# Kernel optimization log

Measured on AMD Instinct MI355X. Metric: run time of the kernel, lower is better.

## Reference

```python
import jax, jax.numpy as jnp
import numpy as np

N_NODES = 100000


def _gcn_norm(edge_index, edge_weight, num_nodes):
    # add self loops with weight 1 (PyG GCNConv default)
    loop = jnp.arange(num_nodes, dtype=edge_index.dtype)
    src = jnp.concatenate([edge_index[0], loop])
    dst = jnp.concatenate([edge_index[1], loop])
    w = jnp.concatenate([edge_weight, jnp.ones(num_nodes, edge_weight.dtype)])
    deg = jax.ops.segment_sum(w, dst, num_segments=num_nodes)
    dinv = jnp.where(deg > 0, jax.lax.rsqrt(deg), 0.0).astype(edge_weight.dtype)
    norm = dinv[src] * w * dinv[dst]
    return src, dst, norm


def _gcn_conv(x, W, b, src, dst, norm):
    h = x @ W                                   # [N, out]
    msg = h[src] * norm[:, None]                # [E+N, out] gather + scale
    out = jax.ops.segment_sum(msg, dst, num_segments=x.shape[0])
    return out + b


def setup_inputs() -> dict:
    key = jax.random.key(0)
    ks = jax.random.split(key, 6)
    nfeat, nhid, nclass, E = 128, 64, 40, 1600000
    return {
        "x": jax.random.normal(ks[0], (N_NODES, nfeat), jnp.float32),
        "edge_index": jax.random.randint(ks[1], (2, E), 0, N_NODES, jnp.int64),
        "edge_weight": jax.random.uniform(ks[2], (E,), jnp.float32),
        "W1": jax.random.normal(ks[3], (nfeat, nhid), jnp.float32) / np.sqrt(nfeat),
        "b1": jnp.zeros((nhid,), jnp.float32),
        "W2": jax.random.normal(ks[4], (nhid, nclass), jnp.float32) / np.sqrt(nhid),
        "b2": jnp.zeros((nclass,), jnp.float32),
    }


def reference(x, edge_index, edge_weight, W1, b1, W2, b2):
    src, dst, norm = _gcn_norm(edge_index, edge_weight, x.shape[0])
    h = jax.nn.relu(_gcn_conv(x, W1, b1, src, dst, norm))
    # dropout p=0.0 / eval mode -> identity
    h = _gcn_conv(h, W2, b2, src, dst, norm)
    return jax.nn.log_softmax(h, axis=1)
```

## Files before the change

kernel.cpp:

```cpp
#include <hip/hip_runtime.h>
#include <hip/hip_fp16.h>
#include <math.h>

#define NFEAT 128
#define NHID 64
#define NCLASS 40
#define BNODES 256
#define BSHIFT 8
#define EPB 4096
#define CAPSH 13
#define CAP (1 << CAPSH)
#define LCAP 5120

typedef _Float16 f16x8 __attribute__((ext_vector_type(8)));
typedef float f32x4 __attribute__((ext_vector_type(4)));

static __device__ __forceinline__ __half2 i2h2(int x) { union { int i; __half2 h; } u; u.i = x; return u.h; }
static __device__ __forceinline__ int h22i(__half2 h) { union { int i; __half2 h; } u; u.h = h; return u.i; }
static __device__ __forceinline__ __half2 shfl_xor_h2(__half2 v, int off) { return i2h2(__shfl_xor(h22i(v), off)); }


__global__ void k_init(int* __restrict__ gcur, int NB) {
    int i = blockIdx.x * blockDim.x + threadIdx.x;
    if (i < NB) gcur[i] = i << CAPSH;
}

__global__ __launch_bounds__(256) void k_bscatter(const int* __restrict__ src, const int* __restrict__ dst,
                                                  const float* __restrict__ w, int* __restrict__ gcur,
                                                  int2* __restrict__ csrT, int E, int NB) {
    __shared__ int lcnt[512], lbase[512], lpos[512];
    int t = threadIdx.x;
    for (int i = t; i < NB; i += 256) { lcnt[i] = 0; lpos[i] = 0; }
    __syncthreads();
    int base = blockIdx.x * EPB;
    int rs[16], rd[16]; float rw[16];
    #pragma unroll
    for (int i = 0; i < 16; i++) {
        int e = base + t + i * 256;
        bool ok = (e < E);
        rd[i] = ok ? dst[e] : -1;
        rs[i] = ok ? src[e] : 0;
        rw[i] = ok ? w[e] : 0.f;
    }
    #pragma unroll
    for (int i = 0; i < 16; i++)
        if (rd[i] >= 0) atomicAdd(&lcnt[rd[i] >> BSHIFT], 1);
    __syncthreads();
    for (int i = t; i < NB; i += 256) if (lcnt[i]) lbase[i] = atomicAdd(&gcur[i], lcnt[i]);
    __syncthreads();
    #pragma unroll
    for (int i = 0; i < 16; i++) {
        if (rd[i] >= 0) {
            int d = rd[i];
            int b = d >> BSHIFT;
            int p = atomicAdd(&lpos[b], 1);
            int2 v;
            v.x = rs[i] | ((d & (BNODES - 1)) << 20);
            v.y = __float_as_int(rw[i]);
            csrT[lbase[b] + p] = v;
        }
    }
}

__global__ __launch_bounds__(512) void k_cscan(const int* __restrict__ gcur, int* __restrict__ cbase, int NB) {
    __shared__ int sh[512];
    int t = threadIdx.x;
    int c = (t < NB) ? (gcur[t] - (t << CAPSH)) : 0;
    sh[t] = c;
    __syncthreads();
    for (int off = 1; off < 512; off <<= 1) {
        int v = (t >= off) ? sh[t - off] : 0;
        __syncthreads();
        sh[t] += v;
        __syncthreads();
    }
    if (t < NB) cbase[t] = sh[t] - c;
}

__global__ __launch_bounds__(256) void k_lsort(const int* __restrict__ gcur, const int* __restrict__ cbase,
                                               const int2* __restrict__ csrT, int2* __restrict__ csr,
                                               int* __restrict__ offs, float* __restrict__ dinv,
                                               int N, int E) {
    __shared__ int2 sorted[LCAP];
    __shared__ int lh[BNODES];
    __shared__ int lo[BNODES];
    __shared__ float da[BNODES];
    int b = blockIdx.x, t = threadIdx.x;
    int rbase = b << CAPSH;
    int cnt = gcur[b] - rbase;
    if (cnt > LCAP) cnt = LCAP;
    int cb = cbase[b];
    lh[t] = 0; da[t] = 0.f;
    __syncthreads();
    int2 reg[20];
    #pragma unroll
    for (int i = 0; i < 20; i++) {
        int e = t + i * 256;
        reg[i] = (e < cnt) ? csrT[rbase + e] : make_int2(-1, 0);
    }
    #pragma unroll
    for (int i = 0; i < 20; i++) {
        if (reg[i].x >= 0) {
            int dl = (reg[i].x >> 20) & 255;
            atomicAdd(&lh[dl], 1);
            atomicAdd(&da[dl], __int_as_float(reg[i].y));
        }
    }
    __syncthreads();
    int own = lh[t];
    lo[t] = own;
    __syncthreads();
    for (int off = 1; off < 256; off <<= 1) {
        int v = (t >= off) ? lo[t - off] : 0;
        __syncthreads();
        lo[t] += v;
        __syncthreads();
    }
    int excl = lo[t] - own;
    __syncthreads();
    lh[t] = excl;
    int gn = (b << BSHIFT) + t;
    if (gn < N) {
        offs[gn] = cb + excl;
        dinv[gn] = rsqrtf(1.0f + da[t]);
    }
    if (b == 0 && t == 0) offs[N] = E;
    __syncthreads();
    #pragma unroll
    for (int i = 0; i < 20; i++) {
        if (reg[i].x >= 0) {
            int dl = (reg[i].x >> 20) & 255;
            int p = atomicAdd(&lh[dl], 1);
            sorted[p] = reg[i];
        }
    }
    __syncthreads();
    for (int e = t; e < cnt; e += 256) {
        int2 v = sorted[e];
        __half2 w2 = __half2half2(__float2half(__int_as_float(v.y)));
        v.x &= 0xFFFFF;
        v.y = h22i(w2);
        csr[cb + e] = v;
    }
}


__global__ __launch_bounds__(256) void k_gemm1(const float* __restrict__ x,
                                               const float* __restrict__ W,
                                               const float* __restrict__ dinv,
                                               __half* __restrict__ h, int N) {
    __shared__ _Float16 xh[64][136];
    __shared__ _Float16 Wt[64][136];
    int t = threadIdx.x;
    int row0 = blockIdx.x * 64;
    for (int i = t; i < 4096; i += 256) {
        int r = i >> 6, k2 = i & 63;
        int row = row0 + r;
        float2 v = (row < N) ? ((const float2*)(x + (size_t)row * NFEAT))[k2]
                             : make_float2(0.f, 0.f);
        *(__half2*)&xh[r][k2 * 2] = __floats2half2_rn(v.x, v.y);
    }
    for (int i = t; i < 4096; i += 256) {
        int k2 = i >> 6, c = i & 63;
        float a0 = W[(size_t)(2 * k2) * NHID + c];
        float a1 = W[(size_t)(2 * k2 + 1) * NHID + c];
        *(__half2*)&Wt[c][k2 * 2] = __floats2half2_rn(a0, a1);
    }
    __syncthreads();
    int wave = t >> 6, lane = t & 63;
    int quad = lane >> 4, l16 = lane & 15;
    int r0 = wave * 16;
    f32x4 acc[4] = {};
    #pragma unroll
    for (int k0 = 0; k0 < 128; k0 += 32) {
        f16x8 af = *(const f16x8*)&xh[r0 + l16][k0 + quad * 8];
        #pragma unroll
        for (int ct = 0; ct < 4; ct++) {
            f16x8 bf = *(const f16x8*)&Wt[ct * 16 + l16][k0 + quad * 8];
            acc[ct] = __builtin_amdgcn_mfma_f32_16x16x32_f16(af, bf, acc[ct], 0, 0, 0);
        }
    }
    #pragma unroll
    for (int ct = 0; ct < 4; ct++) {
        #pragma unroll
        for (int j = 0; j < 4; j++) {
            int row = row0 + r0 + quad * 4 + j;
            if (row < N)
                h[(size_t)row * NHID + ct * 16 + l16] = __float2half(dinv[row] * acc[ct][j]);
        }
    }
}


__global__ __launch_bounds__(256) void k_agg1(const int* __restrict__ offs, const int2* __restrict__ csr,
                                              const __half* __restrict__ h1, const float* __restrict__ dinv,
                                              const float* __restrict__ b1, __half* __restrict__ out1, int N) {
    int n = (blockIdx.x * blockDim.x + threadIdx.x) >> 6;
    if (n >= N) return;
    int lane = threadIdx.x & 63;
    int grp = lane >> 3;
    int c8 = lane & 7;
    const char* hb = (const char*)h1;
    unsigned int c16 = (unsigned int)c8 << 4;
    int e = offs[n], end = offs[n + 1];
    float di = dinv[n];
    float4 hsv = *(const float4*)(hb + (unsigned int)n * 128u + c16);
    float4 bb0 = ((const float4*)b1)[2 * c8];
    float4 bb1 = ((const float4*)b1)[2 * c8 + 1];
    __half2 z = __floats2half2_rn(0.f, 0.f);
    __half2 aA[4] = {z, z, z, z}, aB[4] = {z, z, z, z};
    for (; e + 16 <= end; e += 16) {
        int2 vA = csr[e + grp];
        int2 vB = csr[e + 8 + grp];
        float4 hA = *(const float4*)(hb + (unsigned int)(vA.x & 0xFFFFF) * 128u + c16);
        float4 hB = *(const float4*)(hb + (unsigned int)(vB.x & 0xFFFFF) * 128u + c16);
        __half2 wA = i2h2(vA.y), wB = i2h2(vB.y);
        const __half2* pA = (const __half2*)&hA;
        const __half2* pB = (const __half2*)&hB;
        #pragma unroll
        for (int q = 0; q < 4; q++) {
            aA[q] = __hfma2(wA, pA[q], aA[q]);
            aB[q] = __hfma2(wB, pB[q], aB[q]);
        }
    }
    if (e + 8 <= end) {
        int2 v = csr[e + grp];
        float4 hv = *(const float4*)(hb + (unsigned int)(v.x & 0xFFFFF) * 128u + c16);
        __half2 wv = i2h2(v.y);
        const __half2* p = (const __half2*)&hv;
        #pragma unroll
        for (int q = 0; q < 4; q++) aA[q] = __hfma2(wv, p[q], aA[q]);
        e += 8;
    }
    if (e + grp < end) {
        int2 v = csr[e + grp];
        float4 hv = *(const float4*)(hb + (unsigned int)(v.x & 0xFFFFF) * 128u + c16);
        __half2 wv = i2h2(v.y);
        const __half2* p = (const __half2*)&hv;
        #pragma unroll
        for (int q = 0; q < 4; q++) aB[q] = __hfma2(wv, p[q], aB[q]);
    }
    __half2 acc2[4];
    #pragma unroll
    for (int q = 0; q < 4; q++) acc2[q] = __hadd2(aA[q], aB[q]);
    #pragma unroll
    for (int off = 8; off <= 32; off <<= 1) {
        #pragma unroll
        for (int q = 0; q < 4; q++) acc2[q] = __hadd2(acc2[q], shfl_xor_h2(acc2[q], off));
    }
    if (grp == 0) {
        float a[8], s[8];
        #pragma unroll
        for (int q = 0; q < 4; q++) {
            float2 fa = __half22float2(acc2[q]);
            a[2 * q] = fa.x; a[2 * q + 1] = fa.y;
            float2 f = __half22float2(((const __half2*)&hsv)[q]);
            s[2 * q] = f.x; s[2 * q + 1] = f.y;
        }
        float o[8];
        o[0] = fmaxf(di * (a[0] + s[0]) + bb0.x, 0.f);
        o[1] = fmaxf(di * (a[1] + s[1]) + bb0.y, 0.f);
        o[2] = fmaxf(di * (a[2] + s[2]) + bb0.z, 0.f);
        o[3] = fmaxf(di * (a[3] + s[3]) + bb0.w, 0.f);
        o[4] = fmaxf(di * (a[4] + s[4]) + bb1.x, 0.f);
        o[5] = fmaxf(di * (a[5] + s[5]) + bb1.y, 0.f);
        o[6] = fmaxf(di * (a[6] + s[6]) + bb1.z, 0.f);
        o[7] = fmaxf(di * (a[7] + s[7]) + bb1.w, 0.f);
        float4 st;
        #pragma unroll
        for (int q = 0; q < 4; q++)
            ((__half2*)&st)[q] = __floats2half2_rn(o[2 * q], o[2 * q + 1]);
        ((float4*)out1)[(size_t)n * 8 + c8] = st;
    }
}


__global__ __launch_bounds__(256) void k_gemm2(const __half* __restrict__ a,
                                               const float* __restrict__ W,
                                               const float* __restrict__ dinv,
                                               __half* __restrict__ h, int N) {
    __shared__ _Float16 As[64][72];
    __shared__ _Float16 Bt[64][72];
    int t = threadIdx.x;
    int row0 = blockIdx.x * 64;
    for (int i = t; i < 512; i += 256) {
        int r = i >> 3, q = i & 7;
        int row = row0 + r;
        f16x8 v = {};
        if (row < N) v = *(const f16x8*)(a + (size_t)row * NHID + q * 8);
        *(f16x8*)&As[r][q * 8] = v;
    }
    for (int i = t; i < 4096; i += 256) {
        int c = i >> 6, k = i & 63;
        float wv = (c < NCLASS) ? W[k * NCLASS + c] : 0.f;
        Bt[c][k] = (_Float16)wv;
    }
    __syncthreads();
    int wave = t >> 6, lane = t & 63;
    int quad = lane >> 4, l16 = lane & 15;
    int r0 = wave * 16;
    f32x4 acc[4] = {};
    #pragma unroll
    for (int k0 = 0; k0 < 64; k0 += 32) {
        f16x8 af = *(const f16x8*)&As[r0 + l16][k0 + quad * 8];
        #pragma unroll
        for (int ct = 0; ct < 4; ct++) {
            f16x8 bf = *(const f16x8*)&Bt[ct * 16 + l16][k0 + quad * 8];
            acc[ct] = __builtin_amdgcn_mfma_f32_16x16x32_f16(af, bf, acc[ct], 0, 0, 0);
        }
    }
    #pragma unroll
    for (int ct = 0; ct < 4; ct++) {
        int col = ct * 16 + l16;
        #pragma unroll
        for (int j = 0; j < 4; j++) {
            int row = row0 + r0 + quad * 4 + j;
            if (row < N)
                h[((size_t)row << 6) + col] = __float2half(dinv[row] * acc[ct][j]);
        }
    }
}


__global__ __launch_bounds__(256) void k_agg2(const int* __restrict__ offs, const int2* __restrict__ csr,
                                              const __half* __restrict__ h2, const float* __restrict__ dinv,
                                              const float* __restrict__ b2, float* __restrict__ out, int N) {
    int n = (blockIdx.x * blockDim.x + threadIdx.x) >> 6;
    if (n >= N) return;
    int lane = threadIdx.x & 63;
    int grp = lane >> 3;
    int c8 = lane & 7;
    const char* hb = (const char*)h2;
    unsigned int c16 = (unsigned int)c8 << 4;
    int e = offs[n], end = offs[n + 1];
    bool act = (c8 < 5);
    float di = dinv[n];
    float4 hsv = *(const float4*)(hb + ((unsigned int)n << 7) + c16);
    float4 bb0 = {}, bb1 = {};
    if (act) {
        bb0 = ((const float4*)b2)[2 * c8];
        bb1 = ((const float4*)b2)[2 * c8 + 1];
    }
    __half2 z = __floats2half2_rn(0.f, 0.f);
    __half2 aA[4] = {z, z, z, z}, aB[4] = {z, z, z, z};
    for (; e + 16 <= end; e += 16) {
        int2 vA = csr[e + grp];
        int2 vB = csr[e + 8 + grp];
        float4 hA = *(const float4*)(hb + ((unsigned int)(vA.x & 0xFFFFF) << 7) + c16);
        float4 hB = *(const float4*)(hb + ((unsigned int)(vB.x & 0xFFFFF) << 7) + c16);
        __half2 wA = i2h2(vA.y), wB = i2h2(vB.y);
        const __half2* pA = (const __half2*)&hA;
        const __half2* pB = (const __half2*)&hB;
        #pragma unroll
        for (int q = 0; q < 4; q++) {
            aA[q] = __hfma2(wA, pA[q], aA[q]);
            aB[q] = __hfma2(wB, pB[q], aB[q]);
        }
    }
    if (e + 8 <= end) {
        int2 v = csr[e + grp];
        float4 hv = *(const float4*)(hb + ((unsigned int)(v.x & 0xFFFFF) << 7) + c16);
        __half2 wv = i2h2(v.y);
        const __half2* p = (const __half2*)&hv;
        #pragma unroll
        for (int q = 0; q < 4; q++) aA[q] = __hfma2(wv, p[q], aA[q]);
        e += 8;
    }
    if (e + grp < end) {
        int2 v = csr[e + grp];
        float4 hv = *(const float4*)(hb + ((unsigned int)(v.x & 0xFFFFF) << 7) + c16);
        __half2 wv = i2h2(v.y);
        const __half2* p = (const __half2*)&hv;
        #pragma unroll
        for (int q = 0; q < 4; q++) aB[q] = __hfma2(wv, p[q], aB[q]);
    }
    __half2 acc2[4];
    #pragma unroll
    for (int q = 0; q < 4; q++) acc2[q] = __hadd2(aA[q], aB[q]);
    #pragma unroll
    for (int off = 8; off <= 32; off <<= 1) {
        #pragma unroll
        for (int q = 0; q < 4; q++) acc2[q] = __hadd2(acc2[q], shfl_xor_h2(acc2[q], off));
    }
    float a[8], s[8];
    #pragma unroll
    for (int q = 0; q < 4; q++) {
        float2 fa = __half22float2(acc2[q]);
        a[2 * q] = fa.x; a[2 * q + 1] = fa.y;
        float2 f = __half22float2(((const __half2*)&hsv)[q]);
        s[2 * q] = f.x; s[2 * q + 1] = f.y;
    }
    float v[8];
    v[0] = di * (a[0] + s[0]) + bb0.x;
    v[1] = di * (a[1] + s[1]) + bb0.y;
    v[2] = di * (a[2] + s[2]) + bb0.z;
    v[3] = di * (a[3] + s[3]) + bb0.w;
    v[4] = di * (a[4] + s[4]) + bb1.x;
    v[5] = di * (a[5] + s[5]) + bb1.y;
    v[6] = di * (a[6] + s[6]) + bb1.z;
    v[7] = di * (a[7] + s[7]) + bb1.w;
    float m = -INFINITY;
    if (act) {
        #pragma unroll
        for (int k = 0; k < 8; k++) m = fmaxf(m, v[k]);
    }
    #pragma unroll
    for (int off = 1; off <= 4; off <<= 1) m = fmaxf(m, __shfl_xor(m, off));
    float ex = 0.f;
    if (act) {
        #pragma unroll
        for (int k = 0; k < 8; k++) ex += __expf(v[k] - m);
    }
    #pragma unroll
    for (int off = 1; off <= 4; off <<= 1) ex += __shfl_xor(ex, off);
    if (act && grp == 0) {
        float ls = __logf(ex);
        float4 o0, o1;
        o0.x = v[0] - m - ls; o0.y = v[1] - m - ls; o0.z = v[2] - m - ls; o0.w = v[3] - m - ls;
        o1.x = v[4] - m - ls; o1.y = v[5] - m - ls; o1.z = v[6] - m - ls; o1.w = v[7] - m - ls;
        float* op = out + (size_t)n * NCLASS + c8 * 8;
        *(float4*)op = o0;
        *(float4*)(op + 4) = o1;
    }
}


extern "C" void kernel_launch(void* const* d_in, const int* in_sizes, int n_in,
                              void* d_out, int out_size, void* d_ws, size_t ws_size,
                              hipStream_t stream) {
    const float* x  = (const float*)d_in[0];
    const int*   ei = (const int*)d_in[1];
    const float* w  = (const float*)d_in[2];
    const float* W1 = (const float*)d_in[3];
    const float* b1 = (const float*)d_in[4];
    const float* W2 = (const float*)d_in[5];
    const float* b2 = (const float*)d_in[6];
    float* out = (float*)d_out;

    const int N = in_sizes[0] / NFEAT;
    const int E = in_sizes[1] / 2;
    const int* src = ei;
    const int* dst = ei + E;

    const int NB = (N + BNODES - 1) >> BSHIFT;
    const int nbuild = (E + EPB - 1) / EPB;

    int2*   csrT  = (int2*)d_ws;
    int2*   csr   = csrT + (size_t)NB * CAP;
    float*  dinv  = (float*)(csr + E);
    int*    offs  = (int*)(dinv + N);
    __half* h1h   = (__half*)(offs + N + 1);
    __half* out1h = h1h + (size_t)N * NHID;
    __half* h2old = out1h + (size_t)N * NHID;
    int*    gcur  = (int*)(h2old + (size_t)N * NCLASS);
    int*    cbase = gcur + NB;

    __half* h2p = (__half*)d_ws;

    k_init<<<(NB + 255) / 256, 256, 0, stream>>>(gcur, NB);
    k_bscatter<<<nbuild, 256, 0, stream>>>(src, dst, w, gcur, csrT, E, NB);
    k_cscan<<<1, 512, 0, stream>>>(gcur, cbase, NB);
    k_lsort<<<NB, 256, 0, stream>>>(gcur, cbase, csrT, csr, offs, dinv, N, E);

    k_gemm1<<<(N + 63) / 64, 256, 0, stream>>>(x, W1, dinv, h1h, N);
    k_agg1<<<(N + 3) / 4, 256, 0, stream>>>(offs, csr, h1h, dinv, b1, out1h, N);

    k_gemm2<<<(N + 63) / 64, 256, 0, stream>>>(out1h, W2, dinv, h2p, N);
    k_agg2<<<(N + 3) / 4, 256, 0, stream>>>(offs, csr, h2p, dinv, b2, out, N);
}
```

Measured before the change: 288.1 us.

## Slice layer-1 features into 16-column planes and aggregate each slice separately

k_gemm1 now writes h1 as four column-slice planes of 16 halves per node, [4][N][16], instead of row-major [N][64]. k_agg1 launches four blocks per node group, one per slice, so each gathered row is only 32 bytes and the gather working set per pass is a quarter of the full table, which should raise cache hit rates. Each wave now handles 32 edges per iteration with 2 lanes per edge. CSR entries are read with nontemporal loads. In exchange, the edge list is read four times and the cross-lane reduction has more shuffle steps.

```diff
diff --git a/kernel.cpp b/kernel.cpp
--- a/kernel.cpp
+++ b/kernel.cpp
@@ -11,6 +11,7 @@
 #define CAPSH 13
 #define CAP (1 << CAPSH)
 #define LCAP 5120
+#define NSLICE 4
 
 typedef _Float16 f16x8 __attribute__((ext_vector_type(8)));
 typedef float f32x4 __attribute__((ext_vector_type(4)));
@@ -186,91 +187,75 @@
         for (int j = 0; j < 4; j++) {
             int row = row0 + r0 + quad * 4 + j;
             if (row < N)
-                h[(size_t)row * NHID + ct * 16 + l16] = __float2half(dinv[row] * acc[ct][j]);
+                h[((size_t)ct * N + row) * 16 + l16] = __float2half(dinv[row] * acc[ct][j]);
         }
     }
 }
 
 
 __global__ __launch_bounds__(256) void k_agg1(const int* __restrict__ offs, const int2* __restrict__ csr,
-                                              const __half* __restrict__ h1, const float* __restrict__ dinv,
+                                              const __half* __restrict__ h1s, const float* __restrict__ dinv,
                                               const float* __restrict__ b1, __half* __restrict__ out1, int N) {
-    int n = (blockIdx.x * blockDim.x + threadIdx.x) >> 6;
+    int blk = blockIdx.x;
+    int s = blk & 3;
+    int n = ((blk >> 2) << 2) + (threadIdx.x >> 6);
     if (n >= N) return;
     int lane = threadIdx.x & 63;
-    int grp = lane >> 3;
-    int c8 = lane & 7;
-    const char* hb = (const char*)h1;
-    unsigned int c16 = (unsigned int)c8 << 4;
+    int grp = lane >> 1;
+    int c2 = lane & 1;
+    const char* tb = (const char*)h1s + (size_t)((unsigned)s * (unsigned)N) * 32u;
+    unsigned int coff = (unsigned int)c2 << 4;
     int e = offs[n], end = offs[n + 1];
     float di = dinv[n];
-    float4 hsv = *(const float4*)(hb + (unsigned int)n * 128u + c16);
-    float4 bb0 = ((const float4*)b1)[2 * c8];
-    float4 bb1 = ((const float4*)b1)[2 * c8 + 1];
+    float4 hsv = *(const float4*)(tb + (unsigned int)n * 32u + coff);
+    float4 bb0 = ((const float4*)b1)[s * 4 + c2 * 2];
+    float4 bb1 = ((const float4*)b1)[s * 4 + c2 * 2 + 1];
     __half2 z = __floats2half2_rn(0.f, 0.f);
-    __half2 aA[4] = {z, z, z, z}, aB[4] = {z, z, z, z};
-    for (; e + 16 <= end; e += 16) {
-        int2 vA = csr[e + grp];
-        int2 vB = csr[e + 8 + grp];
-        float4 hA = *(const float4*)(hb + (unsigned int)(vA.x & 0xFFFFF) * 128u + c16);
-        float4 hB = *(const float4*)(hb + (unsigned int)(vB.x & 0xFFFFF) * 128u + c16);
-        __half2 wA = i2h2(vA.y), wB = i2h2(vB.y);
-        const __half2* pA = (const __half2*)&hA;
-        const __half2* pB = (const __half2*)&hB;
+    __half2 acc[4] = {z, z, z, z};
+    for (; e + 32 <= end; e += 32) {
+        long long raw = __builtin_nontemporal_load((const long long*)csr + (e + grp));
+        float4 hv = *(const float4*)(tb + ((unsigned int)((int)raw & 0xFFFFF) << 5) + coff);
+        __half2 wv = i2h2((int)(raw >> 32));
+        const __half2* p = (const __half2*)&hv;
+        #pragma unroll
+        for (int q = 0; q < 4; q++) acc[q] = __hfma2(wv, p[q], acc[q]);
+    }
+    if (e + grp < end) {
+        long long raw = __builtin_nontemporal_load((const long long*)csr + (e + grp));
+        float4 hv = *(const float4*)(tb + ((unsigned int)((int)raw & 0xFFFFF) << 5) + coff);
+        __half2 wv = i2h2((int)(raw >> 32));
+        const __half2* p = (const __half2*)&hv;
+        #pragma unroll
+        for (int q = 0; q < 4; q++) acc[q] = __hfma2(wv, p[q], acc[q]);
+    }
+    #pragma unroll
+    for (int off = 2; off <= 32; off <<= 1) {
+        #pragma unroll
+        for (int q = 0; q < 4; q++) acc[q] = __hadd2(acc[q], shfl_xor_h2(acc[q], off));
+    }
+    if (grp == 0) {
+        float a[8], sv[8];
         #pragma unroll
         for (int q = 0; q < 4; q++) {
-            aA[q] = __hfma2(wA, pA[q], aA[q]);
-            aB[q] = __hfma2(wB, pB[q], aB[q]);
-        }
-    }
-    if (e + 8 <= end) {
-        int2 v = csr[e + grp];
-        float4 hv = *(const float4*)(hb + (unsigned int)(v.x & 0xFFFFF) * 128u + c16);
-        __half2 wv = i2h2(v.y);
-        const __half2* p = (const __half2*)&hv;
-        #pragma unroll
-        for (int q = 0; q < 4; q++) aA[q] = __hfma2(wv, p[q], aA[q]);
-        e += 8;
-    }
-    if (e + grp < end) {
-        int2 v = csr[e + grp];
-        float4 hv = *(const float4*)(hb + (unsigned int)(v.x & 0xFFFFF) * 128u + c16);
-        __half2 wv = i2h2(v.y);
-        const __half2* p = (const __half2*)&hv;
-        #pragma unroll
-        for (int q = 0; q < 4; q++) aB[q] = __hfma2(wv, p[q], aB[q]);
-    }
-    __half2 acc2[4];
-    #pragma unroll
-    for (int q = 0; q < 4; q++) acc2[q] = __hadd2(aA[q], aB[q]);
-    #pragma unroll
-    for (int off = 8; off <= 32; off <<= 1) {
-        #pragma unroll
-        for (int q = 0; q < 4; q++) acc2[q] = __hadd2(acc2[q], shfl_xor_h2(acc2[q], off));
-    }
-    if (grp == 0) {
-        float a[8], s[8];
-        #pragma unroll
-        for (int q = 0; q < 4; q++) {
-            float2 fa = __half22float2(acc2[q]);
+            float2 fa = __half22float2(acc[q]);
             a[2 * q] = fa.x; a[2 * q + 1] = fa.y;
-            float2 f = __half22float2(((const __half2*)&hsv)[q]);
-            s[2 * q] = f.x; s[2 * q + 1] = f.y;
+            float2 fs = __half22float2(((const __half2*)&hsv)[q]);
+            sv[2 * q] = fs.x; sv[2 * q + 1] = fs.y;
         }
         float o[8];
-        o[0] = fmaxf(di * (a[0] + s[0]) + bb0.x, 0.f);
-        o[1] = fmaxf(di * (a[1] + s[1]) + bb0.y, 0.f);
-        o[2] = fmaxf(di * (a[2] + s[2]) + bb0.z, 0.f);
-        o[3] = fmaxf(di * (a[3] + s[3]) + bb0.w, 0.f);
-        o[4] = fmaxf(di * (a[4] + s[4]) + bb1.x, 0.f);
-        o[5] = fmaxf(di * (a[5] + s[5]) + bb1.y, 0.f);
-        o[6] = fmaxf(di * (a[6] + s[6]) + bb1.z, 0.f);
-        o[7] = fmaxf(di * (a[7] + s[7]) + bb1.w, 0.f);
+        o[0] = fmaxf(di * (a[0] + sv[0]) + bb0.x, 0.f);
+        o[1] = fmaxf(di * (a[1] + sv[1]) + bb0.y, 0.f);
+        o[2] = fmaxf(di * (a[2] + sv[2]) + bb0.z, 0.f);
+        o[3] = fmaxf(di * (a[3] + sv[3]) + bb0.w, 0.f);
+        o[4] = fmaxf(di * (a[4] + sv[4]) + bb1.x, 0.f);
+        o[5] = fmaxf(di * (a[5] + sv[5]) + bb1.y, 0.f);
+        o[6] = fmaxf(di * (a[6] + sv[6]) + bb1.z, 0.f);
+        o[7] = fmaxf(di * (a[7] + sv[7]) + bb1.w, 0.f);
         float4 st;
         #pragma unroll
         for (int q = 0; q < 4; q++)
             ((__half2*)&st)[q] = __floats2half2_rn(o[2 * q], o[2 * q + 1]);
-        ((float4*)out1)[(size_t)n * 8 + c8] = st;
+        *(float4*)(out1 + (size_t)n * NHID + s * 16 + c2 * 8) = st;
     }
 }
 
@@ -463,7 +448,7 @@
     k_lsort<<<NB, 256, 0, stream>>>(gcur, cbase, csrT, csr, offs, dinv, N, E);
 
     k_gemm1<<<(N + 63) / 64, 256, 0, stream>>>(x, W1, dinv, h1h, N);
-    k_agg1<<<(N + 3) / 4, 256, 0, stream>>>(offs, csr, h1h, dinv, b1, out1h, N);
+    k_agg1<<<((N + 3) / 4) * NSLICE, 256, 0, stream>>>(offs, csr, h1h, dinv, b1, out1h, N);
 
     k_gemm2<<<(N + 63) / 64, 256, 0, stream>>>(out1h, W2, dinv, h2p, N);
     k_agg2<<<(N + 3) / 4, 256, 0, stream>>>(offs, csr, h2p, dinv, b2, out, N);
```

After: 374.0 us. 1.3x slower.
